# Kernel tuning notes

Hardware: AMD Instinct MI355X
Metric: run time of the kernel (lower is better)

Reference implementation:

```python
import jax, jax.numpy as jnp
import numpy as np

HD = 64        # hidden_dim
H = 4          # heads
N = 50000      # nodes
E = 400000     # edges (before self loops)
NEG_ATT = 0.2  # GATConv attention LeakyReLU slope (PyG default)
NEG_ACT = 0.01 # nn.LeakyReLU() default slope
EPS = 1e-5     # BatchNorm eps


def _bn(x, gamma, beta):
    # training-mode BatchNorm1d over node dimension (biased variance)
    mu = x.mean(0)
    var = x.var(0)
    return gamma * (x - mu) * jax.lax.rsqrt(var + EPS) + beta


def _gatconv(h_in, src, dst, W, a_src, a_dst, bias, heads, outc, concat):
    n = h_in.shape[0]
    h = (h_in @ W.T).reshape(n, heads, outc)              # [N,H,C]
    al_s = jnp.einsum('nhc,hc->nh', h, a_src)             # [N,H]
    al_d = jnp.einsum('nhc,hc->nh', h, a_dst)
    e = jax.nn.leaky_relu(al_s[src] + al_d[dst], NEG_ATT) # [E',H]
    # softmax over incoming edges of each destination node
    m = jax.lax.stop_gradient(jax.ops.segment_max(e, dst, num_segments=n))
    ex = jnp.exp(e - m[dst])
    den = jax.ops.segment_sum(ex, dst, num_segments=n)
    alpha = ex / den[dst]                                  # [E',H]
    out = jax.ops.segment_sum(h[src] * alpha[..., None], dst, num_segments=n)
    out = out.reshape(n, heads * outc) if concat else out.mean(axis=1)
    return out + bias


def setup_inputs() -> dict:
    ks = jax.random.split(jax.random.key(0), 20)
    s = 0.1
    d = {
        'x': jax.random.normal(ks[0], (N, 2 * HD), jnp.float32),
        'edge_index': jax.random.randint(ks[1], (2, E), 0, N, jnp.int64),
        'W1': jax.random.normal(ks[2], (H * HD, 2 * HD), jnp.float32) * s,
        'a1s': jax.random.normal(ks[3], (H, HD), jnp.float32) * s,
        'a1d': jax.random.normal(ks[4], (H, HD), jnp.float32) * s,
        'b1': jnp.zeros((H * HD,), jnp.float32),
        'W2': jax.random.normal(ks[5], (H * HD, H * HD), jnp.float32) * s,
        'a2s': jax.random.normal(ks[6], (H, HD), jnp.float32) * s,
        'a2d': jax.random.normal(ks[7], (H, HD), jnp.float32) * s,
        'b2': jnp.zeros((H * HD,), jnp.float32),
        'W3': jax.random.normal(ks[8], (1 * HD, H * HD), jnp.float32) * s,
        'a3s': jax.random.normal(ks[9], (1, HD), jnp.float32) * s,
        'a3d': jax.random.normal(ks[10], (1, HD), jnp.float32) * s,
        'b3': jnp.zeros((HD,), jnp.float32),
        'gamma': jnp.ones((H * HD,), jnp.float32),
        'beta': jnp.zeros((H * HD,), jnp.float32),
    }
    return d


def reference(x, edge_index, W1, a1s, a1d, b1, W2, a2s, a2d, b2,
              W3, a3s, a3d, b3, gamma, beta):
    n = x.shape[0]
    loop = jnp.arange(n, dtype=edge_index.dtype)
    src = jnp.concatenate([edge_index[0], loop])  # add_self_loops=True
    dst = jnp.concatenate([edge_index[1], loop])

    h = _gatconv(x, src, dst, W1, a1s, a1d, b1, H, HD, True)
    h = jax.nn.leaky_relu(_bn(h, gamma, beta), NEG_ACT)

    # single middle residual block (num_layers=3); dropout is identity (eval)
    res = h
    h = _gatconv(h, src, dst, W2, a2s, a2d, b2, H, HD, True)
    h = jax.nn.leaky_relu(_bn(h, gamma, beta), NEG_ACT)
    h = h + res

    out = _gatconv(h, src, dst, W3, a3s, a3d, b3, 1, HD, False)
    return out
```

## Files before the change

### kernel.cpp

```cpp
#include <hip/hip_runtime.h>
#include <hip/hip_bf16.h>

#define NEG_ATT 0.2f
#define NEG_ACT 0.01f
#define NAGG 2048
#define LOG2E 1.4426950408889634f

typedef __attribute__((ext_vector_type(8))) short short8;
typedef __attribute__((ext_vector_type(4))) float f32x4;

__device__ __forceinline__ float b2f(unsigned short h) {
    return __uint_as_float((unsigned int)h << 16);
}
__device__ __forceinline__ unsigned cvt_pk_bf16(float lo, float hi) {
    unsigned r;
    asm("v_cvt_pk_bf16_f32 %0, %1, %2" : "=v"(r) : "v"(lo), "v"(hi));
    return r;
}
__device__ __forceinline__ float fexp2(float x) {
#if __has_builtin(__builtin_amdgcn_exp2f)
    return __builtin_amdgcn_exp2f(x);
#else
    return exp2f(x);
#endif
}


#define SCAN_CHUNK 1024
__global__ void scan1(const int* __restrict__ deg, int* __restrict__ offs,
                      int* blocksum, int Nn) {
    __shared__ int sh[256];
    int b = blockIdx.x, t = threadIdx.x;
    int base = b * SCAN_CHUNK + t * 4;
    int v[4];
    int s = 0;
    for (int j = 0; j < 4; j++) {
        int idx = base + j;
        v[j] = (idx < Nn) ? deg[idx] + 1 : 0;
        s += v[j];
    }
    sh[t] = s;
    __syncthreads();
    for (int off = 1; off < 256; off <<= 1) {
        int x = (t >= off) ? sh[t - off] : 0;
        __syncthreads();
        sh[t] += x;
        __syncthreads();
    }
    int excl = sh[t] - s;
    if (t == 255) blocksum[b] = sh[255];
    int run = excl;
    for (int j = 0; j < 4; j++) {
        int idx = base + j;
        if (idx < Nn) offs[idx] = run;
        run += v[j];
    }
}

__global__ void scan23(int* __restrict__ offs, const int* __restrict__ bsum,
                       int* __restrict__ cursor, int Nn, int G) {
    int i = blockIdx.x * 256 + threadIdx.x;
    if (i > Nn) return;
    int g = i >> 10;
    int basev = 0;
    for (int k = 0; k < g; k++) basev += bsum[k];
    if (i == Nn) {
        int tot = basev;
        for (int k = g; k < G; k++) tot += bsum[k];
        offs[Nn] = tot;
        return;
    }
    int v = offs[i] + basev;
    offs[i] = v;
    cursor[i] = v;
}

__global__ void fill_csr(const int* __restrict__ ei, int* cursor, int* csr, int E, int Nn) {
    int t = blockIdx.x * 256 + threadIdx.x;
    if (t < E) {
        int s = ei[t];
        int d = ei[E + t];
        int p = atomicAdd(&cursor[d], 1);
        csr[p] = s;
    } else if (t < E + Nn) {
        int nn = t - E;
        int p = atomicAdd(&cursor[nn], 1);
        csr[p] = nn;
    }
}


__global__ __launch_bounds__(256) void prep_all(
    int* __restrict__ deg, const int* __restrict__ ei, int E,
    const float* __restrict__ x, unsigned short* __restrict__ xb, int nx, int nxpad,
    const float* __restrict__ w1, unsigned short* __restrict__ o1, int n1,
    const float* __restrict__ w2, unsigned short* __restrict__ o2, int n2,
    const float* __restrict__ w3, unsigned short* __restrict__ o3, int n3) {
    int id = blockIdx.x * 256 + threadIdx.x;
    int nconv = (nxpad + n1 + n2 + n3) / 8;
    if (id >= nconv) {
        int e = id - nconv;
        if (e < E) atomicAdd(&deg[ei[E + e]], 1);
        return;
    }
    int i = id * 8;
    const float* in;
    unsigned short* out;
    if (i < nxpad) {
        if (i >= nx) {
            *(ushort4*)&xb[i] = make_ushort4(0, 0, 0, 0);
            *(ushort4*)&xb[i + 4] = make_ushort4(0, 0, 0, 0);
            return;
        }
        in = x + i; out = xb + i;
    } else {
        int j = i - nxpad;
        if (j < n1) { in = w1 + j; out = o1 + j; }
        else if (j < n1 + n2) { in = w2 + (j - n1); out = o2 + (j - n1); }
        else { in = w3 + (j - n1 - n2); out = o3 + (j - n1 - n2); }
    }
    float4 a = *(const float4*)in;
    float4 b = *(const float4*)(in + 4);
    uint4 o;
    o.x = cvt_pk_bf16(a.x, a.y);
    o.y = cvt_pk_bf16(a.z, a.w);
    o.z = cvt_pk_bf16(b.x, b.y);
    o.w = cvt_pk_bf16(b.z, b.w);
    *(uint4*)out = o;
}

template <bool RES>
__device__ __forceinline__ unsigned bnpack2(unsigned short ya, unsigned short yb_,
                                            float sca, float scb, float sha, float shb,
                                            unsigned short ra, unsigned short rb_) {
    float v0 = sca * b2f(ya) + sha; v0 = v0 > 0.f ? v0 : NEG_ACT * v0;
    float v1 = scb * b2f(yb_) + shb; v1 = v1 > 0.f ? v1 : NEG_ACT * v1;
    if (RES) { v0 += b2f(ra); v1 += b2f(rb_); }
    return cvt_pk_bf16(v0, v1);
}


template <int K, int CO, int HEADS, bool FUSE, bool FRES, bool FWOUT>
__global__ __launch_bounds__(256) void gemm_mfma(
    const unsigned short* __restrict__ Xb, const unsigned short* __restrict__ Wb,
    unsigned short* __restrict__ Hb, const float* __restrict__ a_s,
    const float* __restrict__ a_d, float* __restrict__ als, float* __restrict__ ald,
    const unsigned short* __restrict__ Yb_in, unsigned short* __restrict__ RWbuf,
    const float* __restrict__ scale, const float* __restrict__ shift, int Nn) {
    constexpr int BM = 128, BK = 64, LD = 72, SLD = 68;
    __shared__ __align__(16) char smem[4 * 32 * SLD * 4];
    unsigned short* As = (unsigned short*)smem;
    unsigned short* Bs = As + BM * LD;
    int tid = threadIdx.x;
    int wave = tid >> 6, lane = tid & 63;
    int quad = lane >> 4, l16 = lane & 15;
    int mt, hd;
    if (HEADS == 4) {
        int gm = gridDim.x >> 2;
        int gm8 = gm & ~7;
        int nfull = gm8 * 4;
        int id = blockIdx.x;
        if (id < nfull) {
            int r = id & 31;
            mt = (id >> 5) * 8 + (r & 7);
            hd = r >> 3;
        } else {
            int t2 = id - nfull;
            mt = gm8 + (t2 >> 2);
            hd = t2 & 3;
        }
    } else {
        mt = blockIdx.x;
        hd = 0;
    }
    int m0 = mt * BM, n0 = hd * 64;
    int arow = tid >> 3;
    int achk = (tid & 7) * 8;
    f32x4 acc[2][4] = {};
    for (int k0 = 0; k0 < K; k0 += BK) {
        __syncthreads();
        if (FUSE) {
            int cb = k0 + achk;
            float4 sc0 = *(const float4*)&scale[cb];
            float4 sc1 = *(const float4*)&scale[cb + 4];
            float4 sh0 = *(const float4*)&shift[cb];
            float4 sh1 = *(const float4*)&shift[cb + 4];
#pragma unroll
            for (int p = 0; p < 4; p++) {
                int r = arow + p * 32;
                int m = m0 + r;
                uint4 o = make_uint4(0, 0, 0, 0);
                if (m < Nn) {
                    ushort4 ua = *(const ushort4*)&Yb_in[(size_t)m * 256 + cb];
                    ushort4 ub = *(const ushort4*)&Yb_in[(size_t)m * 256 + cb + 4];
                    ushort4 ra = make_ushort4(0, 0, 0, 0), rb = ra;
                    if (FRES) {
                        ra = *(const ushort4*)&RWbuf[(size_t)m * 256 + cb];
                        rb = *(const ushort4*)&RWbuf[(size_t)m * 256 + cb + 4];
                    }
                    o.x = bnpack2<FRES>(ua.x, ua.y, sc0.x, sc0.y, sh0.x, sh0.y, ra.x, ra.y);
                    o.y = bnpack2<FRES>(ua.z, ua.w, sc0.z, sc0.w, sh0.z, sh0.w, ra.z, ra.w);
                    o.z = bnpack2<FRES>(ub.x, ub.y, sc1.x, sc1.y, sh1.x, sh1.y, rb.x, rb.y);
                    o.w = bnpack2<FRES>(ub.z, ub.w, sc1.z, sc1.w, sh1.z, sh1.w, rb.z, rb.w);
                    if (FWOUT && hd == 0)
                        *(uint4*)&RWbuf[(size_t)m * 256 + cb] = o;
                }
                *(uint4*)&As[r * LD + achk] = o;
            }
        } else {
#pragma unroll
            for (int p = 0; p < 4; p++) {
                int r = arow + p * 32;
                *(int4*)&As[r * LD + achk] = *(const int4*)&Xb[(size_t)(m0 + r) * K + k0 + achk];
            }
        }
#pragma unroll
        for (int p = 0; p < 2; p++) {
            int r = arow + p * 32;
            *(int4*)&Bs[r * LD + achk] = *(const int4*)&Wb[(size_t)(n0 + r) * K + k0 + achk];
        }
        __syncthreads();
#pragma unroll
        for (int ks = 0; ks < 2; ks++) {
            short8 af[2], bfr[4];
#pragma unroll
            for (int i = 0; i < 2; i++)
                af[i] = *(const short8*)&As[(wave * 32 + i * 16 + l16) * LD + ks * 32 + quad * 8];
#pragma unroll
            for (int j = 0; j < 4; j++)
                bfr[j] = *(const short8*)&Bs[(j * 16 + l16) * LD + ks * 32 + quad * 8];
#pragma unroll
            for (int i = 0; i < 2; i++)
#pragma unroll
                for (int j = 0; j < 4; j++)
                    acc[i][j] = __builtin_amdgcn_mfma_f32_16x16x32_bf16(af[i], bfr[j], acc[i][j], 0, 0, 0);
        }
    }
    __syncthreads();

    float asv[4], adv[4];
#pragma unroll
    for (int j = 0; j < 4; j++) {
        asv[j] = a_s[hd * 64 + j * 16 + l16] * LOG2E;
        adv[j] = a_d[hd * 64 + j * 16 + l16] * LOG2E;
    }
#pragma unroll
    for (int i = 0; i < 2; i++)
#pragma unroll
        for (int r = 0; r < 4; r++) {
            float ps = acc[i][0][r] * asv[0] + acc[i][1][r] * asv[1] +
                       acc[i][2][r] * asv[2] + acc[i][3][r] * asv[3];
            float pd = acc[i][0][r] * adv[0] + acc[i][1][r] * adv[1] +
                       acc[i][2][r] * adv[2] + acc[i][3][r] * adv[3];
#pragma unroll
            for (int mm = 1; mm < 16; mm <<= 1) {
                ps += __shfl_xor(ps, mm);
                pd += __shfl_xor(pd, mm);
            }
            if (l16 == 0) {
                int m = m0 + wave * 32 + i * 16 + quad * 4 + r;
                als[m * HEADS + hd] = ps;
                ald[m * HEADS + hd] = pd;
            }
        }

    float* stg = (float*)smem + wave * 32 * SLD;
#pragma unroll
    for (int i = 0; i < 2; i++)
#pragma unroll
        for (int j = 0; j < 4; j++)
#pragma unroll
            for (int r = 0; r < 4; r++)
                stg[(i * 16 + quad * 4 + r) * SLD + j * 16 + l16] = acc[i][j][r];
    int g = lane >> 3, c8 = (lane & 7) * 8;
#pragma unroll
    for (int p = 0; p < 4; p++) {
        int row = p * 8 + g;
        float4 v0 = *(const float4*)&stg[row * SLD + c8];
        float4 v1 = *(const float4*)&stg[row * SLD + c8 + 4];
        uint4 o;
        o.x = cvt_pk_bf16(v0.x, v0.y);
        o.y = cvt_pk_bf16(v0.z, v0.w);
        o.z = cvt_pk_bf16(v1.x, v1.y);
        o.w = cvt_pk_bf16(v1.z, v1.w);
        *(uint4*)&Hb[(size_t)(m0 + wave * 32 + row) * CO + n0 + c8] = o;
    }
}


#define EDGE4(J)                                                                     \
    {                                                                                \
        int s0 = __builtin_amdgcn_readlane(idx, (J));                                \
        int s1 = __builtin_amdgcn_readlane(idx, (J) + 1);                            \
        int s2 = __builtin_amdgcn_readlane(idx, (J) + 2);                            \
        int s3 = __builtin_amdgcn_readlane(idx, (J) + 3);                            \
        const unsigned short* r0 = Hb + (size_t)s0 * 256;                            \
        const unsigned short* r1 = Hb + (size_t)s1 * 256;                            \
        const unsigned short* r2 = Hb + (size_t)s2 * 256;                            \
        const unsigned short* r3 = Hb + (size_t)s3 * 256;                            \
        float a0 = als[s0 * 4 + hd], a1 = als[s1 * 4 + hd];                          \
        float a2 = als[s2 * 4 + hd], a3 = als[s3 * 4 + hd];                          \
        ushort4 h0 = *(const ushort4*)&r0[c4];                                       \
        ushort4 h1 = *(const ushort4*)&r1[c4];                                       \
        ushort4 h2 = *(const ushort4*)&r2[c4];                                       \
        ushort4 h3 = *(const ushort4*)&r3[c4];                                       \
        float e0 = a0 + aldn; e0 = fmaxf(e0, NEG_ATT * e0);                          \
        float e1 = a1 + aldn; e1 = fmaxf(e1, NEG_ATT * e1);                          \
        float e2 = a2 + aldn; e2 = fmaxf(e2, NEG_ATT * e2);                          \
        float e3 = a3 + aldn; e3 = fmaxf(e3, NEG_ATT * e3);                          \
        float w0 = fexp2(e0), w1 = fexp2(e1), w2 = fexp2(e2), w3 = fexp2(e3);        \
        den += (w0 + w1) + (w2 + w3);                                                \
        acc.x += w0 * b2f(h0.x) + w1 * b2f(h1.x) + w2 * b2f(h2.x) + w3 * b2f(h3.x);  \
        acc.y += w0 * b2f(h0.y) + w1 * b2f(h1.y) + w2 * b2f(h2.y) + w3 * b2f(h3.y);  \
        acc.z += w0 * b2f(h0.z) + w1 * b2f(h1.z) + w2 * b2f(h2.z) + w3 * b2f(h3.z);  \
        acc.w += w0 * b2f(h0.w) + w1 * b2f(h1.w) + w2 * b2f(h2.w) + w3 * b2f(h3.w);  \
    }

__global__ __launch_bounds__(256) void aggregate_h4(
    const unsigned short* __restrict__ Hb, const float* __restrict__ als,
    const float* __restrict__ ald, const int* __restrict__ offs,
    const int* __restrict__ csr, unsigned short* __restrict__ Yb,
    float* __restrict__ partial, int Nn) {
    __shared__ float red[4 * 512];
    int wave = threadIdx.x >> 6;
    int lane = threadIdx.x & 63;
    int hd = lane >> 4;
    int c4 = lane * 4;
    float4 bs = make_float4(0.f, 0.f, 0.f, 0.f);
    float4 bq = make_float4(0.f, 0.f, 0.f, 0.f);
    for (int n = blockIdx.x * 4 + wave; n < Nn; n += gridDim.x * 4) {
        float aldn = ald[n * 4 + hd];
        int beg = __builtin_amdgcn_readfirstlane(offs[n]);
        int end = __builtin_amdgcn_readfirstlane(offs[n + 1]);
        float4 acc = make_float4(0.f, 0.f, 0.f, 0.f);
        float den = 0.f;
        for (int b = beg; b < end; b += 64) {
            int cnt = min(64, end - b);
            int idx = 0;
            if (lane < cnt) idx = csr[b + lane];
            int j = 0;
            for (; j + 8 <= cnt; j += 8) {
                EDGE4(j);
                EDGE4(j + 4);
            }
            for (; j + 4 <= cnt; j += 4) {
                EDGE4(j);
            }
            for (; j < cnt; j++) {
                int s = __builtin_amdgcn_readlane(idx, j);
                const unsigned short* rr = Hb + (size_t)s * 256;
                float e = als[s * 4 + hd] + aldn;
                e = fmaxf(e, NEG_ATT * e);
                float w = fexp2(e);
                den += w;
                ushort4 hv = *(const ushort4*)&rr[c4];
                acc.x += w * b2f(hv.x); acc.y += w * b2f(hv.y);
                acc.z += w * b2f(hv.z); acc.w += w * b2f(hv.w);
            }
        }
        float inv = 1.f / den;
        float yx = acc.x * inv, yy = acc.y * inv, yz = acc.z * inv, yw = acc.w * inv;
        uint2 o;
        o.x = cvt_pk_bf16(yx, yy);
        o.y = cvt_pk_bf16(yz, yw);
        *(uint2*)&Yb[(size_t)n * 256 + c4] = o;
        bs.x += yx; bs.y += yy; bs.z += yz; bs.w += yw;
        bq.x += yx * yx; bq.y += yy * yy; bq.z += yz * yz; bq.w += yw * yw;
    }
    float* rs = &red[wave * 512];
    rs[c4 + 0] = bs.x; rs[c4 + 1] = bs.y; rs[c4 + 2] = bs.z; rs[c4 + 3] = bs.w;
    rs[256 + c4 + 0] = bq.x; rs[256 + c4 + 1] = bq.y;
    rs[256 + c4 + 2] = bq.z; rs[256 + c4 + 3] = bq.w;
    __syncthreads();
    int t = threadIdx.x;
    float v0 = red[t] + red[512 + t] + red[1024 + t] + red[1536 + t];
    float v1 = red[256 + t] + red[768 + t] + red[1280 + t] + red[1792 + t];
    partial[(size_t)blockIdx.x * 512 + t] = v0;
    partial[(size_t)blockIdx.x * 512 + 256 + t] = v1;
}

__global__ __launch_bounds__(256) void bn_combine(const float* __restrict__ partial,
                                                  float* __restrict__ S) {
    int t = threadIdx.x;
    int b0 = blockIdx.x * (NAGG / 32);
    float s0 = 0.f, s1 = 0.f;
#pragma unroll 8
    for (int b = b0; b < b0 + NAGG / 32; b++) {
        s0 += partial[(size_t)b * 512 + t];
        s1 += partial[(size_t)b * 512 + 256 + t];
    }
    atomicAdd(&S[t], s0);
    atomicAdd(&S[256 + t], s1);
}

__global__ __launch_bounds__(256) void aggregate_h1(
    const unsigned short* __restrict__ Hb, const float* __restrict__ als,
    const float* __restrict__ ald, const int* __restrict__ offs,
    const int* __restrict__ csr, const float* __restrict__ bias,
    float* __restrict__ Yout, int Nn) {
    int wave = threadIdx.x >> 6;
    int lane = threadIdx.x & 63;
    int sub = lane >> 4, lane16 = lane & 15;
    int n = blockIdx.x * 16 + wave * 4 + sub;
    if (n >= Nn) return;
    int c4 = lane16 * 4;
    float aldn = ald[n];
    int beg = offs[n], end = offs[n + 1];
    float4 acc = make_float4(0.f, 0.f, 0.f, 0.f);
    float den = 0.f;
    for (int b = beg; b < end; b += 16) {
        int cnt = min(16, end - b);
        int idx = 0;
        if (lane16 < cnt) idx = csr[b + lane16];
        int j = 0;
        for (; j + 4 <= cnt; j += 4) {
            int s0 = __shfl(idx, (sub << 4) + j);
            int s1 = __shfl(idx, (sub << 4) + j + 1);
            int s2 = __shfl(idx, (sub << 4) + j + 2);
            int s3 = __shfl(idx, (sub << 4) + j + 3);
            float a0 = als[s0], a1 = als[s1], a2 = als[s2], a3 = als[s3];
            ushort4 h0 = *(const ushort4*)&Hb[(size_t)s0 * 64 + c4];
            ushort4 h1 = *(const ushort4*)&Hb[(size_t)s1 * 64 + c4];
            ushort4 h2 = *(const ushort4*)&Hb[(size_t)s2 * 64 + c4];
            ushort4 h3 = *(const ushort4*)&Hb[(size_t)s3 * 64 + c4];
            float e0 = a0 + aldn; e0 = fmaxf(e0, NEG_ATT * e0);
            float e1 = a1 + aldn; e1 = fmaxf(e1, NEG_ATT * e1);
            float e2 = a2 + aldn; e2 = fmaxf(e2, NEG_ATT * e2);
            float e3 = a3 + aldn; e3 = fmaxf(e3, NEG_ATT * e3);
            float w0 = fexp2(e0), w1 = fexp2(e1), w2 = fexp2(e2), w3 = fexp2(e3);
            den += (w0 + w1) + (w2 + w3);
            acc.x += w0 * b2f(h0.x) + w1 * b2f(h1.x) + w2 * b2f(h2.x) + w3 * b2f(h3.x);
            acc.y += w0 * b2f(h0.y) + w1 * b2f(h1.y) + w2 * b2f(h2.y) + w3 * b2f(h3.y);
            acc.z += w0 * b2f(h0.z) + w1 * b2f(h1.z) + w2 * b2f(h2.z) + w3 * b2f(h3.z);
            acc.w += w0 * b2f(h0.w) + w1 * b2f(h1.w) + w2 * b2f(h2.w) + w3 * b2f(h3.w);
        }
        for (; j < cnt; j++) {
            int s = __shfl(idx, (sub << 4) + j);
            float e = als[s] + aldn;
            e = fmaxf(e, NEG_ATT * e);
            float w = fexp2(e);
            den += w;
            ushort4 hv = *(const ushort4*)&Hb[(size_t)s * 64 + c4];
            acc.x += w * b2f(hv.x); acc.y += w * b2f(hv.y);
            acc.z += w * b2f(hv.z); acc.w += w * b2f(hv.w);
        }
    }
    float inv = 1.f / den;
    float4 bv = *(const float4*)&bias[c4];
    float4 o = make_float4(acc.x * inv + bv.x, acc.y * inv + bv.y,
                           acc.z * inv + bv.z, acc.w * inv + bv.w);
    *(float4*)&Yout[(size_t)n * 64 + c4] = o;
}


__global__ __launch_bounds__(256) void bn_final(
    const float* __restrict__ S, const float* __restrict__ gamma,
    const float* __restrict__ beta, float* __restrict__ scale,
    float* __restrict__ shift, float inv_n) {
    int ch = threadIdx.x;
    float mu = S[ch] * inv_n;
    float var = S[256 + ch] * inv_n - mu * mu;
    float sc = gamma[ch] * rsqrtf(var + 1e-5f);
    scale[ch] = sc;
    shift[ch] = beta[ch] - mu * sc;
}


extern "C" void kernel_launch(void* const* d_in, const int* in_sizes, int n_in,
                              void* d_out, int out_size, void* d_ws, size_t ws_size,
                              hipStream_t stream) {
    const float* x    = (const float*)d_in[0];
    const int*   ei   = (const int*)d_in[1];
    const float* W1   = (const float*)d_in[2];
    const float* a1s  = (const float*)d_in[3];
    const float* a1d  = (const float*)d_in[4];
    const float* W2   = (const float*)d_in[6];
    const float* a2s  = (const float*)d_in[7];
    const float* a2d  = (const float*)d_in[8];
    const float* W3   = (const float*)d_in[10];
    const float* a3s  = (const float*)d_in[11];
    const float* a3d  = (const float*)d_in[12];
    const float* b3   = (const float*)d_in[13];
    const float* gamma = (const float*)d_in[14];
    const float* beta  = (const float*)d_in[15];
    float* out = (float*)d_out;

    const int Nn = in_sizes[0] / 128;
    const int E  = in_sizes[1] / 2;
    const int Ep = E + Nn;
    const int Mpad = (Nn + 127) & ~127;

    size_t off = 0;
    char* base = (char*)d_ws;
    auto alloc = [&](size_t bytes) -> void* {
        void* p = base + off;
        off = (off + bytes + 255) & ~(size_t)255;
        return p;
    };
    unsigned short* Hb   = (unsigned short*)alloc((size_t)Mpad * 256 * 2);
    unsigned short* Yb   = (unsigned short*)alloc((size_t)Nn * 256 * 2);
    unsigned short* xb1  = (unsigned short*)alloc((size_t)Mpad * 128 * 2);
    unsigned short* xbig = (unsigned short*)alloc((size_t)Mpad * 256 * 2);
    unsigned short* wb1  = (unsigned short*)alloc((size_t)256 * 128 * 2);
    unsigned short* wb2  = (unsigned short*)alloc((size_t)256 * 256 * 2);
    unsigned short* wb3  = (unsigned short*)alloc((size_t)64 * 256 * 2);
    float* als    = (float*)alloc((size_t)Mpad * 4 * 4);
    float* ald    = (float*)alloc((size_t)Mpad * 4 * 4);
    size_t zoff0 = off;
    int*   deg    = (int*)alloc((size_t)Nn * 4);
    float* sums   = (float*)alloc(1024 * 4);
    size_t zbytes = off - zoff0;
    int*   offs   = (int*)alloc((size_t)(Nn + 1) * 4);
    int*   cursor = (int*)alloc((size_t)Nn * 4);
    int*   bsum   = (int*)alloc(64 * 4);
    int*   csr    = (int*)alloc((size_t)Ep * 4);
    float* partial = (float*)alloc((size_t)NAGG * 512 * 4);
    float* scale  = (float*)alloc(256 * 4);
    float* shift  = (float*)alloc(256 * 4);
    (void)ws_size;

    float* sums0 = sums;
    float* sums1 = sums + 512;

    const int G = (Nn + SCAN_CHUNK - 1) / SCAN_CHUNK;

    hipMemsetAsync(deg, 0, zbytes, stream);
    {
        int nxpad = Mpad * 128;
        int wtot = 256 * 128 + 256 * 256 + 64 * 256;
        int nconv = (nxpad + wtot) / 8;
        prep_all<<<(nconv + E + 255) / 256, 256, 0, stream>>>(
            deg, ei, E, x, xb1, Nn * 128, nxpad,
            W1, wb1, 256 * 128, W2, wb2, 256 * 256, W3, wb3, 64 * 256);
    }

    scan1<<<G, 256, 0, stream>>>(deg, offs, bsum, Nn);
    scan23<<<(Nn + 1 + 255) / 256, 256, 0, stream>>>(offs, bsum, cursor, Nn, G);
    fill_csr<<<(Ep + 255) / 256, 256, 0, stream>>>(ei, cursor, csr, E, Nn);

    const int gm = Mpad / 128;
    const int nagg1 = (Nn + 15) / 16;
    const float inv_n = 1.f / (float)Nn;

    gemm_mfma<128, 256, 4, false, false, false><<<gm * 4, 256, 0, stream>>>(
        xb1, wb1, Hb, a1s, a1d, als, ald, nullptr, nullptr, nullptr, nullptr, 0);
    aggregate_h4<<<NAGG, 256, 0, stream>>>(Hb, als, ald, offs, csr, Yb, partial, Nn);
    bn_combine<<<32, 256, 0, stream>>>(partial, sums0);
    bn_final<<<1, 256, 0, stream>>>(sums0, gamma, beta, scale, shift, inv_n);

    gemm_mfma<256, 256, 4, true, false, true><<<gm * 4, 256, 0, stream>>>(
        nullptr, wb2, Hb, a2s, a2d, als, ald, Yb, xbig, scale, shift, Nn);
    aggregate_h4<<<NAGG, 256, 0, stream>>>(Hb, als, ald, offs, csr, Yb, partial, Nn);
    bn_combine<<<32, 256, 0, stream>>>(partial, sums1);
    bn_final<<<1, 256, 0, stream>>>(sums1, gamma, beta, scale, shift, inv_n);

    gemm_mfma<256, 64, 1, true, true, false><<<gm, 256, 0, stream>>>(
        nullptr, wb3, Hb, a3s, a3d, als, ald, Yb, xbig, scale, shift, Nn);
    aggregate_h1<<<nagg1, 256, 0, stream>>>(Hb, als, ald, offs, csr, b3, out, Nn);
}
```

Baseline: 331.7 us.

## Compute all four heads per block in new gemm_h4 kernel

Adds a gemm_h4 kernel in which each 64-row block computes all 256 output columns, with one wave per head, instead of launching four blocks per 128-row tile (one per head). The A tile, including the fused BatchNorm/LeakyReLU transform and residual write, is loaded and transformed once per row tile rather than four times. The output is staged through shared memory for coalesced bf16 stores. In exchange it loads the full 256-row weight tile per k-step, uses a larger accumulator array per wave, and has fewer resident blocks, which may lower occupancy.

```diff
diff --git a/kernel.cpp b/kernel.cpp
--- a/kernel.cpp
+++ b/kernel.cpp
@@ -137,6 +137,148 @@
     float v1 = scb * b2f(yb_) + shb; v1 = v1 > 0.f ? v1 : NEG_ACT * v1;
     if (RES) { v0 += b2f(ra); v1 += b2f(rb_); }
     return cvt_pk_bf16(v0, v1);
+}
+
+
+template <int K, bool FUSE, bool FRES, bool FWOUT>
+__global__ __launch_bounds__(256) void gemm_h4(
+    const unsigned short* __restrict__ Xb, const unsigned short* __restrict__ Wb,
+    unsigned short* __restrict__ Hb, const float* __restrict__ a_s,
+    const float* __restrict__ a_d, float* __restrict__ als, float* __restrict__ ald,
+    const unsigned short* __restrict__ Yb_in, unsigned short* __restrict__ RWbuf,
+    const float* __restrict__ scale, const float* __restrict__ shift, int Nn) {
+    constexpr int LD = 72;
+    constexpr int SP = 268;
+    __shared__ __align__(16) char smem[(64 + 256) * LD * 2];
+    unsigned short* As = (unsigned short*)smem;
+    unsigned short* Bs = As + 64 * LD;
+    int tid = threadIdx.x;
+    int hd = tid >> 6;
+    int lane = tid & 63;
+    int quad = lane >> 4, l16 = lane & 15;
+    int m0 = blockIdx.x * 64;
+    int arow = tid >> 3;
+    int achk = (tid & 7) * 8;
+    f32x4 acc[4][4] = {};
+    for (int k0 = 0; k0 < K; k0 += 64) {
+        __syncthreads();
+        if (FUSE) {
+            int cb = k0 + achk;
+            float4 sc0 = *(const float4*)&scale[cb];
+            float4 sc1 = *(const float4*)&scale[cb + 4];
+            float4 sh0 = *(const float4*)&shift[cb];
+            float4 sh1 = *(const float4*)&shift[cb + 4];
+#pragma unroll
+            for (int p = 0; p < 2; p++) {
+                int r = arow + p * 32;
+                int m = m0 + r;
+                uint4 o = make_uint4(0, 0, 0, 0);
+                if (m < Nn) {
+                    ushort4 ua = *(const ushort4*)&Yb_in[(size_t)m * 256 + cb];
+                    ushort4 ub = *(const ushort4*)&Yb_in[(size_t)m * 256 + cb + 4];
+                    ushort4 ra = make_ushort4(0, 0, 0, 0), rb = ra;
+                    if (FRES) {
+                        ra = *(const ushort4*)&RWbuf[(size_t)m * 256 + cb];
+                        rb = *(const ushort4*)&RWbuf[(size_t)m * 256 + cb + 4];
+                    }
+                    o.x = bnpack2<FRES>(ua.x, ua.y, sc0.x, sc0.y, sh0.x, sh0.y, ra.x, ra.y);
+                    o.y = bnpack2<FRES>(ua.z, ua.w, sc0.z, sc0.w, sh0.z, sh0.w, ra.z, ra.w);
+                    o.z = bnpack2<FRES>(ub.x, ub.y, sc1.x, sc1.y, sh1.x, sh1.y, rb.x, rb.y);
+                    o.w = bnpack2<FRES>(ub.z, ub.w, sc1.z, sc1.w, sh1.z, sh1.w, rb.z, rb.w);
+                    if (FWOUT)
+                        *(uint4*)&RWbuf[(size_t)m * 256 + cb] = o;
+                }
+                *(uint4*)&As[r * LD + achk] = o;
+            }
+        } else {
+#pragma unroll
+            for (int p = 0; p < 2; p++) {
+                int r = arow + p * 32;
+                *(int4*)&As[r * LD + achk] = *(const int4*)&Xb[(size_t)(m0 + r) * K + k0 + achk];
+            }
+        }
+#pragma unroll
+        for (int p = 0; p < 8; p++) {
+            int r = arow + p * 32;
+            *(int4*)&Bs[r * LD + achk] = *(const int4*)&Wb[(size_t)r * K + k0 + achk];
+        }
+        __syncthreads();
+#pragma unroll
+        for (int ks = 0; ks < 2; ks++) {
+            short8 af[4], bfr[4];
+#pragma unroll
+            for (int i = 0; i < 4; i++)
+                af[i] = *(const short8*)&As[(i * 16 + l16) * LD + ks * 32 + quad * 8];
+#pragma unroll
+            for (int j = 0; j < 4; j++)
+                bfr[j] = *(const short8*)&Bs[(hd * 64 + j * 16 + l16) * LD + ks * 32 + quad * 8];
+#pragma unroll
+            for (int i = 0; i < 4; i++)
+#pragma unroll
+                for (int j = 0; j < 4; j++)
+                    acc[i][j] = __builtin_amdgcn_mfma_f32_16x16x32_bf16(af[i], bfr[j], acc[i][j], 0, 0, 0);
+        }
+    }
+    __syncthreads();
+
+    float asv[4], adv[4];
+#pragma unroll
+    for (int j = 0; j < 4; j++) {
+        asv[j] = a_s[hd * 64 + j * 16 + l16] * LOG2E;
+        adv[j] = a_d[hd * 64 + j * 16 + l16] * LOG2E;
+    }
+#pragma unroll
+    for (int i = 0; i < 4; i++)
+#pragma unroll
+        for (int r = 0; r < 4; r++) {
+            float ps = acc[i][0][r] * asv[0] + acc[i][1][r] * asv[1] +
+                       acc[i][2][r] * asv[2] + acc[i][3][r] * asv[3];
+            float pd = acc[i][0][r] * adv[0] + acc[i][1][r] * adv[1] +
+                       acc[i][2][r] * adv[2] + acc[i][3][r] * adv[3];
+#pragma unroll
+            for (int mm = 1; mm < 16; mm <<= 1) {
+                ps += __shfl_xor(ps, mm);
+                pd += __shfl_xor(pd, mm);
+            }
+            if (l16 == 0) {
+                int m = m0 + i * 16 + quad * 4 + r;
+                als[m * 4 + hd] = ps;
+                ald[m * 4 + hd] = pd;
+            }
+        }
+
+    float* stg = (float*)smem;
+#pragma unroll
+    for (int ph = 0; ph < 2; ph++) {
+        __syncthreads();
+#pragma unroll
+        for (int i2 = 0; i2 < 2; i2++) {
+            int i = ph * 2 + i2;
+#pragma unroll
+            for (int j = 0; j < 4; j++) {
+                int c = hd * 64 + j * 16 + l16;
+                int cs = c + (c >> 5);
+#pragma unroll
+                for (int r = 0; r < 4; r++)
+                    stg[(i2 * 16 + quad * 4 + r) * SP + cs] = acc[i][j][r];
+            }
+        }
+        __syncthreads();
+        int row = tid >> 3;
+        int cch = (tid & 7) * 32;
+        const float4* sp = (const float4*)&stg[row * SP + cch + (cch >> 5)];
+        uint4* dst = (uint4*)&Hb[(size_t)(m0 + ph * 32 + row) * 256 + cch];
+#pragma unroll
+        for (int q = 0; q < 4; q++) {
+            float4 va = sp[2 * q], vb = sp[2 * q + 1];
+            uint4 o;
+            o.x = cvt_pk_bf16(va.x, va.y);
+            o.y = cvt_pk_bf16(va.z, va.w);
+            o.z = cvt_pk_bf16(vb.x, vb.y);
+            o.w = cvt_pk_bf16(vb.z, vb.w);
+            dst[q] = o;
+        }
+    }
 }
 
 
@@ -154,26 +296,8 @@
     int tid = threadIdx.x;
     int wave = tid >> 6, lane = tid & 63;
     int quad = lane >> 4, l16 = lane & 15;
-    int mt, hd;
-    if (HEADS == 4) {
-        int gm = gridDim.x >> 2;
-        int gm8 = gm & ~7;
-        int nfull = gm8 * 4;
-        int id = blockIdx.x;
-        if (id < nfull) {
-            int r = id & 31;
-            mt = (id >> 5) * 8 + (r & 7);
-            hd = r >> 3;
-        } else {
-            int t2 = id - nfull;
-            mt = gm8 + (t2 >> 2);
-            hd = t2 & 3;
-        }
-    } else {
-        mt = blockIdx.x;
-        hd = 0;
-    }
-    int m0 = mt * BM, n0 = hd * 64;
+    int mt = blockIdx.x, hd = 0;
+    int m0 = mt * BM, n0 = 0;
     int arow = tid >> 3;
     int achk = (tid & 7) * 8;
     f32x4 acc[2][4] = {};
@@ -217,7 +341,8 @@
 #pragma unroll
         for (int p = 0; p < 2; p++) {
             int r = arow + p * 32;
-            *(int4*)&Bs[r * LD + achk] = *(const int4*)&Wb[(size_t)(n0 + r) * K + k0 + achk];
+            if (r < CO)
+                *(int4*)&Bs[r * LD + achk] = *(const int4*)&Wb[(size_t)(n0 + r) * K + k0 + achk];
         }
         __syncthreads();
 #pragma unroll
@@ -241,8 +366,8 @@
     float asv[4], adv[4];
 #pragma unroll
     for (int j = 0; j < 4; j++) {
-        asv[j] = a_s[hd * 64 + j * 16 + l16] * LOG2E;
-        adv[j] = a_d[hd * 64 + j * 16 + l16] * LOG2E;
+        asv[j] = a_s[j * 16 + l16] * LOG2E;
+        adv[j] = a_d[j * 16 + l16] * LOG2E;
     }
 #pragma unroll
     for (int i = 0; i < 2; i++)
@@ -538,17 +663,18 @@
     scan23<<<(Nn + 1 + 255) / 256, 256, 0, stream>>>(offs, bsum, cursor, Nn, G);
     fill_csr<<<(Ep + 255) / 256, 256, 0, stream>>>(ei, cursor, csr, E, Nn);
 
-    const int gm = Mpad / 128;
+    const int gm  = Mpad / 128;
+    const int gm4 = Mpad / 64;
     const int nagg1 = (Nn + 15) / 16;
     const float inv_n = 1.f / (float)Nn;
 
-    gemm_mfma<128, 256, 4, false, false, false><<<gm * 4, 256, 0, stream>>>(
-        xb1, wb1, Hb, a1s, a1d, als, ald, nullptr, nullptr, nullptr, nullptr, 0);
+    gemm_h4<128, false, false, false><<<gm4, 256, 0, stream>>>(
+        xb1, wb1, Hb, a1s, a1d, als, ald, nullptr, nullptr, nullptr, nullptr, Nn);
     aggregate_h4<<<NAGG, 256, 0, stream>>>(Hb, als, ald, offs, csr, Yb, partial, Nn);
     bn_combine<<<32, 256, 0, stream>>>(partial, sums0);
     bn_final<<<1, 256, 0, stream>>>(sums0, gamma, beta, scale, shift, inv_n);
 
-    gemm_mfma<256, 256, 4, true, false, true><<<gm * 4, 256, 0, stream>>>(
+    gemm_h4<256, true, false, true><<<gm4, 256, 0, stream>>>(
         nullptr, wb2, Hb, a2s, a2d, als, ald, Yb, xbig, scale, shift, Nn);
     aggregate_h4<<<NAGG, 256, 0, stream>>>(Hb, als, ald, offs, csr, Yb, partial, Nn);
     bn_combine<<<32, 256, 0, stream>>>(partial, sums1);
```

Result: slower. 357.5 us (+7.7%).

## Split BN statistics out of aggregation into separate stats and reduce kernels

Applied to the files above, without the earlier changes.

Removes the fused BatchNorm sum/sumsq accumulation from the 4-head aggregation kernel, which now launches one wave per node instead of a fixed 2048-block grid-stride loop. A new bn_stats kernel rereads the bf16 aggregated output to compute per-block partials. A per-channel bn_reduce_final kernel then reduces them and computes scale/shift, replacing the atomic combine and the zeroed sums buffer. This simplifies the aggregation kernel and its scheduling at the cost of an extra full read of the output per layer. Stats are now taken from bf16-rounded values.

```diff
diff --git a/kernel.cpp b/kernel.cpp
--- a/kernel.cpp
+++ b/kernel.cpp
@@ -3,7 +3,6 @@
 
 #define NEG_ATT 0.2f
 #define NEG_ACT 0.01f
-#define NAGG 2048
 #define LOG2E 1.4426950408889634f
 
 typedef __attribute__((ext_vector_type(8))) short short8;
@@ -319,78 +318,47 @@
 __global__ __launch_bounds__(256) void aggregate_h4(
     const unsigned short* __restrict__ Hb, const float* __restrict__ als,
     const float* __restrict__ ald, const int* __restrict__ offs,
-    const int* __restrict__ csr, unsigned short* __restrict__ Yb,
-    float* __restrict__ partial, int Nn) {
-    __shared__ float red[4 * 512];
+    const int* __restrict__ csr, unsigned short* __restrict__ Yb, int Nn) {
     int wave = threadIdx.x >> 6;
     int lane = threadIdx.x & 63;
+    int n = blockIdx.x * 4 + wave;
+    if (n >= Nn) return;
     int hd = lane >> 4;
     int c4 = lane * 4;
-    float4 bs = make_float4(0.f, 0.f, 0.f, 0.f);
-    float4 bq = make_float4(0.f, 0.f, 0.f, 0.f);
-    for (int n = blockIdx.x * 4 + wave; n < Nn; n += gridDim.x * 4) {
-        float aldn = ald[n * 4 + hd];
-        int beg = __builtin_amdgcn_readfirstlane(offs[n]);
-        int end = __builtin_amdgcn_readfirstlane(offs[n + 1]);
-        float4 acc = make_float4(0.f, 0.f, 0.f, 0.f);
-        float den = 0.f;
-        for (int b = beg; b < end; b += 64) {
-            int cnt = min(64, end - b);
-            int idx = 0;
-            if (lane < cnt) idx = csr[b + lane];
-            int j = 0;
-            for (; j + 8 <= cnt; j += 8) {
-                EDGE4(j);
-                EDGE4(j + 4);
-            }
-            for (; j + 4 <= cnt; j += 4) {
-                EDGE4(j);
-            }
-            for (; j < cnt; j++) {
-                int s = __builtin_amdgcn_readlane(idx, j);
-                const unsigned short* rr = Hb + (size_t)s * 256;
-                float e = als[s * 4 + hd] + aldn;
-                e = fmaxf(e, NEG_ATT * e);
-                float w = fexp2(e);
-                den += w;
-                ushort4 hv = *(const ushort4*)&rr[c4];
-                acc.x += w * b2f(hv.x); acc.y += w * b2f(hv.y);
-                acc.z += w * b2f(hv.z); acc.w += w * b2f(hv.w);
-            }
-        }
-        float inv = 1.f / den;
-        float yx = acc.x * inv, yy = acc.y * inv, yz = acc.z * inv, yw = acc.w * inv;
-        uint2 o;
-        o.x = cvt_pk_bf16(yx, yy);
-        o.y = cvt_pk_bf16(yz, yw);
-        *(uint2*)&Yb[(size_t)n * 256 + c4] = o;
-        bs.x += yx; bs.y += yy; bs.z += yz; bs.w += yw;
-        bq.x += yx * yx; bq.y += yy * yy; bq.z += yz * yz; bq.w += yw * yw;
-    }
-    float* rs = &red[wave * 512];
-    rs[c4 + 0] = bs.x; rs[c4 + 1] = bs.y; rs[c4 + 2] = bs.z; rs[c4 + 3] = bs.w;
-    rs[256 + c4 + 0] = bq.x; rs[256 + c4 + 1] = bq.y;
-    rs[256 + c4 + 2] = bq.z; rs[256 + c4 + 3] = bq.w;
-    __syncthreads();
-    int t = threadIdx.x;
-    float v0 = red[t] + red[512 + t] + red[1024 + t] + red[1536 + t];
-    float v1 = red[256 + t] + red[768 + t] + red[1280 + t] + red[1792 + t];
-    partial[(size_t)blockIdx.x * 512 + t] = v0;
-    partial[(size_t)blockIdx.x * 512 + 256 + t] = v1;
-}
-
-__global__ __launch_bounds__(256) void bn_combine(const float* __restrict__ partial,
-                                                  float* __restrict__ S) {
-    int t = threadIdx.x;
-    int b0 = blockIdx.x * (NAGG / 32);
-    float s0 = 0.f, s1 = 0.f;
-#pragma unroll 8
-    for (int b = b0; b < b0 + NAGG / 32; b++) {
-        s0 += partial[(size_t)b * 512 + t];
-        s1 += partial[(size_t)b * 512 + 256 + t];
-    }
-    atomicAdd(&S[t], s0);
-    atomicAdd(&S[256 + t], s1);
+    float aldn = ald[n * 4 + hd];
+    int beg = __builtin_amdgcn_readfirstlane(offs[n]);
+    int end = __builtin_amdgcn_readfirstlane(offs[n + 1]);
+    float4 acc = make_float4(0.f, 0.f, 0.f, 0.f);
+    float den = 0.f;
+    for (int b = beg; b < end; b += 64) {
+        int cnt = min(64, end - b);
+        int idx = 0;
+        if (lane < cnt) idx = csr[b + lane];
+        int j = 0;
+        for (; j + 8 <= cnt; j += 8) {
+            EDGE4(j);
+            EDGE4(j + 4);
+        }
+        for (; j + 4 <= cnt; j += 4) {
+            EDGE4(j);
+        }
+        for (; j < cnt; j++) {
+            int s = __builtin_amdgcn_readlane(idx, j);
+            const unsigned short* rr = Hb + (size_t)s * 256;
+            float e = als[s * 4 + hd] + aldn;
+            e = fmaxf(e, NEG_ATT * e);
+            float w = fexp2(e);
+            den += w;
+            ushort4 hv = *(const ushort4*)&rr[c4];
+            acc.x += w * b2f(hv.x); acc.y += w * b2f(hv.y);
+            acc.z += w * b2f(hv.z); acc.w += w * b2f(hv.w);
+        }
+    }
+    float inv = 1.f / den;
+    uint2 o;
+    o.x = cvt_pk_bf16(acc.x * inv, acc.y * inv);
+    o.y = cvt_pk_bf16(acc.z * inv, acc.w * inv);
+    *(uint2*)&Yb[(size_t)n * 256 + c4] = o;
 }
 
 __global__ __launch_bounds__(256) void aggregate_h1(
@@ -453,16 +421,63 @@
 }
 
 
-__global__ __launch_bounds__(256) void bn_final(
-    const float* __restrict__ S, const float* __restrict__ gamma,
-    const float* __restrict__ beta, float* __restrict__ scale,
-    float* __restrict__ shift, float inv_n) {
-    int ch = threadIdx.x;
-    float mu = S[ch] * inv_n;
-    float var = S[256 + ch] * inv_n - mu * mu;
-    float sc = gamma[ch] * rsqrtf(var + 1e-5f);
-    scale[ch] = sc;
-    shift[ch] = beta[ch] - mu * sc;
+__global__ __launch_bounds__(256) void bn_stats(const unsigned short* __restrict__ Yb,
+                                                float* __restrict__ partial, int Nn) {
+    __shared__ float red[4 * 512];
+    int t = threadIdx.x;
+    int g = blockIdx.x;
+    int rows_per = (Nn + gridDim.x - 1) / gridDim.x;
+    int r0 = g * rows_per;
+    int r1 = min(r0 + rows_per, Nn);
+    int sub = t >> 6;
+    int c4 = (t & 63) * 4;
+    float4 s = make_float4(0.f, 0.f, 0.f, 0.f);
+    float4 q = make_float4(0.f, 0.f, 0.f, 0.f);
+    for (int r = r0 + sub; r < r1; r += 4) {
+        ushort4 u = *(const ushort4*)&Yb[(size_t)r * 256 + c4];
+        float vx = b2f(u.x), vy = b2f(u.y), vz = b2f(u.z), vw = b2f(u.w);
+        s.x += vx; s.y += vy; s.z += vz; s.w += vw;
+        q.x += vx * vx; q.y += vy * vy; q.z += vz * vz; q.w += vw * vw;
+    }
+    float* rs = &red[sub * 512];
+    rs[c4 + 0] = s.x; rs[c4 + 1] = s.y; rs[c4 + 2] = s.z; rs[c4 + 3] = s.w;
+    rs[256 + c4 + 0] = q.x; rs[256 + c4 + 1] = q.y;
+    rs[256 + c4 + 2] = q.z; rs[256 + c4 + 3] = q.w;
+    __syncthreads();
+    float v0 = red[t] + red[512 + t] + red[1024 + t] + red[1536 + t];
+    float v1 = red[256 + t] + red[768 + t] + red[1280 + t] + red[1792 + t];
+    partial[(size_t)g * 512 + t] = v0;
+    partial[(size_t)g * 512 + 256 + t] = v1;
+}
+
+__global__ __launch_bounds__(256) void bn_reduce_final(
+    const float* __restrict__ partial, int NP, const float* __restrict__ gamma,
+    const float* __restrict__ beta, float* scale, float* shift, int Nn) {
+    __shared__ float sh[8];
+    int ch = blockIdx.x;
+    int t = threadIdx.x;
+    int wave = t >> 6, lane = t & 63;
+    float s = 0.f, q = 0.f;
+    for (int i = t; i < NP; i += 256) {
+        s += partial[(size_t)i * 512 + ch];
+        q += partial[(size_t)i * 512 + 256 + ch];
+    }
+    for (int off = 32; off; off >>= 1) {
+        s += __shfl_down(s, off);
+        q += __shfl_down(q, off);
+    }
+    if (lane == 0) { sh[wave] = s; sh[4 + wave] = q; }
+    __syncthreads();
+    if (t == 0) {
+        s = sh[0] + sh[1] + sh[2] + sh[3];
+        q = sh[4] + sh[5] + sh[6] + sh[7];
+        float inv_n = 1.f / (float)Nn;
+        float mu = s * inv_n;
+        float var = q * inv_n - mu * mu;
+        float sc = gamma[ch] * rsqrtf(var + 1e-5f);
+        scale[ch] = sc;
+        shift[ch] = beta[ch] - mu * sc;
+    }
 }
 
 
@@ -506,25 +521,20 @@
     unsigned short* wb3  = (unsigned short*)alloc((size_t)64 * 256 * 2);
     float* als    = (float*)alloc((size_t)Mpad * 4 * 4);
     float* ald    = (float*)alloc((size_t)Mpad * 4 * 4);
-    size_t zoff0 = off;
     int*   deg    = (int*)alloc((size_t)Nn * 4);
-    float* sums   = (float*)alloc(1024 * 4);
-    size_t zbytes = off - zoff0;
     int*   offs   = (int*)alloc((size_t)(Nn + 1) * 4);
     int*   cursor = (int*)alloc((size_t)Nn * 4);
     int*   bsum   = (int*)alloc(64 * 4);
     int*   csr    = (int*)alloc((size_t)Ep * 4);
-    float* partial = (float*)alloc((size_t)NAGG * 512 * 4);
+    const int NP = 1024;
+    float* partial = (float*)alloc((size_t)NP * 512 * 4);
     float* scale  = (float*)alloc(256 * 4);
     float* shift  = (float*)alloc(256 * 4);
     (void)ws_size;
 
-    float* sums0 = sums;
-    float* sums1 = sums + 512;
-
     const int G = (Nn + SCAN_CHUNK - 1) / SCAN_CHUNK;
 
-    hipMemsetAsync(deg, 0, zbytes, stream);
+    hipMemsetAsync(deg, 0, (size_t)Nn * 4, stream);
     {
         int nxpad = Mpad * 128;
         int wtot = 256 * 128 + 256 * 256 + 64 * 256;
@@ -539,20 +549,20 @@
     fill_csr<<<(Ep + 255) / 256, 256, 0, stream>>>(ei, cursor, csr, E, Nn);
 
     const int gm = Mpad / 128;
+    const int nagg4 = (Nn + 3) / 4;
     const int nagg1 = (Nn + 15) / 16;
-    const float inv_n = 1.f / (float)Nn;
 
     gemm_mfma<128, 256, 4, false, false, false><<<gm * 4, 256, 0, stream>>>(
         xb1, wb1, Hb, a1s, a1d, als, ald, nullptr, nullptr, nullptr, nullptr, 0);
-    aggregate_h4<<<NAGG, 256, 0, stream>>>(Hb, als, ald, offs, csr, Yb, partial, Nn);
-    bn_combine<<<32, 256, 0, stream>>>(partial, sums0);
-    bn_final<<<1, 256, 0, stream>>>(sums0, gamma, beta, scale, shift, inv_n);
+    aggregate_h4<<<nagg4, 256, 0, stream>>>(Hb, als, ald, offs, csr, Yb, Nn);
+    bn_stats<<<NP, 256, 0, stream>>>(Yb, partial, Nn);
+    bn_reduce_final<<<256, 256, 0, stream>>>(partial, NP, gamma, beta, scale, shift, Nn);
 
     gemm_mfma<256, 256, 4, true, false, true><<<gm * 4, 256, 0, stream>>>(
         nullptr, wb2, Hb, a2s, a2d, als, ald, Yb, xbig, scale, shift, Nn);
-    aggregate_h4<<<NAGG, 256, 0, stream>>>(Hb, als, ald, offs, csr, Yb, partial, Nn);
-    bn_combine<<<32, 256, 0, stream>>>(partial, sums1);
-    bn_final<<<1, 256, 0, stream>>>(sums1, gamma, beta, scale, shift, inv_n);
+    aggregate_h4<<<nagg4, 256, 0, stream>>>(Hb, als, ald, offs, csr, Yb, Nn);
+    bn_stats<<<NP, 256, 0, stream>>>(Yb, partial, Nn);
+    bn_reduce_final<<<256, 256, 0, stream>>>(partial, NP, gamma, beta, scale, shift, Nn);
 
     gemm_mfma<256, 64, 1, true, true, false><<<gm, 256, 0, stream>>>(
         nullptr, wb3, Hb, a3s, a3d, als, ald, Yb, xbig, scale, shift, Nn);
```

Result: faster. 325.1 us (-2.0%).
